# Kernel optimization log

Measured on AMD Instinct MI355X. Metric: run time of the kernel, lower is better.

Reference implementation:

```python
import jax, jax.numpy as jnp
import numpy as np
from jax import lax

DN = ('NHWC', 'HWIO', 'NHWC')


def conv2d(x, w, b):
    y = lax.conv_general_dilated(x, w, window_strides=(1, 1), padding='SAME',
                                 dimension_numbers=DN)
    return y + b


def setup_inputs() -> dict:
    key = jax.random.key(0)
    ks = jax.random.split(key, 9)
    C = 256
    NA, NC = 9, 80
    inp = {
        'x0': jax.random.normal(ks[0], (8, 128, 128, C), jnp.float32),
        'x1': jax.random.normal(ks[1], (8, 64, 64, C), jnp.float32),
        'x2': jax.random.normal(ks[2], (8, 32, 32, C), jnp.float32),
        # 4 intermediate 3x3 conv layers per branch (Conv2DNorm: conv -> relu)
        'cls_w': jax.random.normal(ks[3], (4, 3, 3, C, C), jnp.float32) * 0.05,
        'cls_b': jnp.zeros((4, C), jnp.float32),
        'bbox_w': jax.random.normal(ks[4], (4, 3, 3, C, C), jnp.float32) * 0.05,
        'bbox_b': jnp.zeros((4, C), jnp.float32),
        # final prediction convs (no activation)
        'cls_out_w': jax.random.normal(ks[5], (3, 3, C, NA * NC), jnp.float32) * 0.01,
        'cls_out_b': jnp.full((NA * NC,), -np.log((1 - 0.01) / 0.01), jnp.float32),
        'bbox_out_w': jax.random.normal(ks[6], (3, 3, C, NA * 4), jnp.float32) * 0.01,
        'bbox_out_b': jax.random.normal(ks[7], (NA * 4,), jnp.float32) * 0.01,
    }
    return inp


def _forward_single(x, cls_w, cls_b, bbox_w, bbox_b,
                    cls_out_w, cls_out_b, bbox_out_w, bbox_out_b):
    cls_score = x
    bbox_pred = x
    for i in range(cls_w.shape[0]):  # num_heads = 4, structurally fixed
        cls_score = jax.nn.relu(conv2d(cls_score, cls_w[i], cls_b[i]))
        bbox_pred = jax.nn.relu(conv2d(bbox_pred, bbox_w[i], bbox_b[i]))
    cls_score = conv2d(cls_score, cls_out_w, cls_out_b)
    bbox_pred = conv2d(bbox_pred, bbox_out_w, bbox_out_b)
    return cls_score, bbox_pred


def reference(x0, x1, x2, cls_w, cls_b, bbox_w, bbox_b,
              cls_out_w, cls_out_b, bbox_out_w, bbox_out_b):
    cls_scores, bbox_preds = [], []
    for x in (x0, x1, x2):  # pyramid levels (fixed, structurally distinct shapes)
        c, b = _forward_single(x, cls_w, cls_b, bbox_w, bbox_b,
                               cls_out_w, cls_out_b, bbox_out_w, bbox_out_b)
        cls_scores.append(c)
        bbox_preds.append(b)
    return (*cls_scores, *bbox_preds)
```

## Files before the change

### kernel.cpp

```cpp
#include <hip/hip_runtime.h>
#include <stdint.h>

typedef __attribute__((ext_vector_type(8))) short bf16x8;
typedef __attribute__((ext_vector_type(4))) float f32x4;
typedef __attribute__((ext_vector_type(4))) unsigned int u32x4;

__device__ __forceinline__ unsigned short f2bf(float f) {
  unsigned int u = __float_as_uint(f);
  return (unsigned short)((u + 0x7fffu + ((u >> 16) & 1u)) >> 16);
}

__device__ __forceinline__ void gload16(const void* g, void* l) {
  __builtin_amdgcn_global_load_lds((const __attribute__((address_space(1))) void*)g,
                                   (__attribute__((address_space(3))) void*)l, 16, 0, 0);
}

__global__ void zero_k(u32x4* __restrict__ p, int n16) {
  int i = blockIdx.x * blockDim.x + threadIdx.x;
  int stride = gridDim.x * blockDim.x;
  u32x4 z = {0u, 0u, 0u, 0u};
  for (; i < n16; i += stride) p[i] = z;
}

__global__ void conv_in_k(const float* __restrict__ x, unsigned short* __restrict__ dst,
                          int H, int total) {
  int idx = blockIdx.x * 256 + threadIdx.x;
  if (idx >= total) return;
  const int W = H, Hp = H + 2, Wp = H + 2;
  int c8 = idx & 31;
  int rest = idx >> 5;
  int xp = rest % Wp;
  int r2 = rest / Wp;
  int yp = r2 % Hp;
  int n = r2 / Hp;
  u32x4 o = {0u, 0u, 0u, 0u};
  int iy = yp - 1, ix = xp - 1;
  if ((unsigned)iy < (unsigned)H && (unsigned)ix < (unsigned)W) {
    const float* s = x + ((long)((n * H + iy) * W + ix) * 256 + c8 * 8);
    float4 a = *(const float4*)s;
    float4 b = *(const float4*)(s + 4);
    o.x = f2bf(a.x) | ((unsigned)f2bf(a.y) << 16);
    o.y = f2bf(a.z) | ((unsigned)f2bf(a.w) << 16);
    o.z = f2bf(b.x) | ((unsigned)f2bf(b.y) << 16);
    o.w = f2bf(b.z) | ((unsigned)f2bf(b.w) << 16);
  }
  *(u32x4*)(dst + (long)idx * 8) = o;
}

__global__ void conv_w_k(const float* __restrict__ w, unsigned short* __restrict__ wTf,
                         int CoutReal, int NB, int totalChunks) {
  int f = blockIdx.x * 256 + threadIdx.x;
  if (f >= totalChunks) return;
  int l = f & 63;
  int t2 = f >> 6;
  int ks = t2 & 1;
  int t3 = t2 >> 1;
  int jg = t3 % NB;
  int stage = t3 / NB;
  int col = jg * 16 + (l & 15);
  int kbase = stage * 64 + ks * 32 + ((l >> 4) << 3);
  u32x4 o = {0u, 0u, 0u, 0u};
  if (col < CoutReal) {
    unsigned short v[8];
#pragma unroll
    for (int e = 0; e < 8; ++e)
      v[e] = f2bf(w[(long)(kbase + e) * CoutReal + col]);
    o.x = v[0] | ((unsigned)v[1] << 16);
    o.y = v[2] | ((unsigned)v[3] << 16);
    o.z = v[4] | ((unsigned)v[5] << 16);
    o.w = v[6] | ((unsigned)v[7] << 16);
  }
  *(u32x4*)(wTf + (long)f * 8) = o;
}

template<int NF, bool FINAL>
__global__ __launch_bounds__(256, 2)
void conv3x3_k(const unsigned short* __restrict__ src,
               const unsigned short* __restrict__ wTf,
               const float* __restrict__ bias,
               unsigned short* __restrict__ dstAct,
               float* __restrict__ dstOut,
               int H, int lntx, int lnty, int CoutReal, int NB)
{
  __shared__ char smem[49152];
  const int tid = threadIdx.x;
  const int W = H, Hp = H + 2, RL = H + 2;
  const int np = gridDim.x;
  const int bx = blockIdx.x;
  const int t = (bx & 7) * (np >> 3) + (bx >> 3);
  const int tx = (t & ((1 << lntx) - 1)) << 4;
  const int ty = ((t >> lntx) & ((1 << lnty) - 1)) << 3;
  const int n_img = t >> (lntx + lnty);
  const int tileN = blockIdx.y * (NF * 32);

  int srcOff[6];
#pragma unroll
  for (int j = 0; j < 6; ++j) {
    int q = j * 256 + tid;
    int hr = q >> 3, c = q & 7;
    if (hr >= 180) hr = 0;
    int hy = hr / 18, hx = hr - hy * 18;
    int lch = c ^ (hr & 7);
    srcOff[j] = ((n_img * Hp + ty + hy) * RL + tx + hx) * 256 + lch * 8;
  }

  const int lane = tid & 63;
  const int wv = tid >> 6;
  const int l15 = lane & 15;
  const int k8 = lane >> 4;
  const int pxRow = (wv & 1) * 4;
  const int jgBase = (tileN >> 4) + (wv >> 1) * NF;
  const unsigned short* wBp = wTf + (size_t)jgBase * 1024 + lane * 8;
  const size_t stageStride = (size_t)NB << 10;

  int rBase[4];
#pragma unroll
  for (int m = 0; m < 4; ++m)
    rBase[m] = (pxRow + m) * 18 + l15;

  f32x4 acc[4][NF];
#pragma unroll
  for (int m = 0; m < 4; ++m)
#pragma unroll
    for (int n = 0; n < NF; ++n)
      acc[m][n] = (f32x4){0.f, 0.f, 0.f, 0.f};

  auto loadB = [&](bf16x8 (&dst)[NF][2], int stage) {
    const unsigned short* bp = wBp + stage * stageStride;
#pragma unroll
    for (int n = 0; n < NF; ++n)
#pragma unroll
      for (int ks = 0; ks < 2; ++ks)
        dst[n][ks] = *(const bf16x8*)(bp + n * 1024 + ks * 512);
  };
  auto loadAm = [&](bf16x8 (&dst)[2], const char* buf, int tap, int m) {
    const int ky = tap / 3, kx = tap - ky * 3;
    const int rA = rBase[m] + ky * 18 + kx;
    const int a0 = rA * 128 + ((k8 ^ (rA & 7)) << 4);
    dst[0] = *(const bf16x8*)(buf + a0);
    dst[1] = *(const bf16x8*)(buf + (a0 ^ 64));
  };

  bf16x8 avr[4][2];
  bf16x8 bb[2][NF][2];
  loadB(bb[0], 0);

#pragma unroll
  for (int j = 0; j < 6; ++j)
    gload16(src + srcOff[j], smem + j * 4096 + tid * 16);
  __syncthreads();
#pragma unroll
  for (int m = 0; m < 4; ++m)
    loadAm(avr[m], smem, 0, m);

#pragma unroll
  for (int cc = 0; cc < 4; ++cc) {
    char* cbuf = smem + (cc & 1) * 24576;
    if (cc < 3) {
      char* nbuf = smem + ((cc + 1) & 1) * 24576;
#pragma unroll
      for (int j = 0; j < 6; ++j)
        gload16(src + srcOff[j] + (cc + 1) * 64, nbuf + j * 4096 + tid * 16);
    }
#pragma unroll
    for (int tap = 0; tap < 9; ++tap) {
      const int s = cc * 9 + tap;
      const int cur = s & 1, nxt = cur ^ 1;
      if (cc < 3 || tap < 8)
        loadB(bb[nxt], (tap < 8) ? ((tap + 1) * 4 + cc) : (cc + 1));
      __builtin_amdgcn_s_setprio(1);
#pragma unroll
      for (int m = 0; m < 4; ++m) {
#pragma unroll
        for (int n = 0; n < NF; ++n) {
          acc[m][n] = __builtin_amdgcn_mfma_f32_16x16x32_bf16(avr[m][0], bb[cur][n][0], acc[m][n], 0, 0, 0);
          acc[m][n] = __builtin_amdgcn_mfma_f32_16x16x32_bf16(avr[m][1], bb[cur][n][1], acc[m][n], 0, 0, 0);
        }
        if (tap < 8)
          loadAm(avr[m], cbuf, tap + 1, m);
      }
      __builtin_amdgcn_s_setprio(0);
    }
    __syncthreads();
    if (cc < 3) {
      const char* nbuf = smem + ((cc + 1) & 1) * 24576;
#pragma unroll
      for (int m = 0; m < 4; ++m)
        loadAm(avr[m], nbuf, 0, m);
    }
  }

  if constexpr (FINAL) {
    constexpr int NCOL = NF * 32;
    constexpr int MASK = NCOL / 4 - 1;
    float* cf = (float*)smem;
#pragma unroll
    for (int h = 0; h < 2; ++h) {
      if (h) __syncthreads();
      if ((wv & 1) == h) {
#pragma unroll
        for (int n = 0; n < NF; ++n) {
          const int col = (wv >> 1) * (NF * 16) + n * 16 + l15;
          const int colG = tileN + col;
          const float bvl = (colG < CoutReal) ? bias[colG] : 0.f;
          const int c32 = col >> 2;
#pragma unroll
          for (int m = 0; m < 4; ++m)
#pragma unroll
            for (int r = 0; r < 4; ++r) {
              const int pxl = m * 16 + (k8 << 2) + r;
              const int phys = (c32 + (k8 & 1) * 4) & MASK;
              cf[pxl * NCOL + phys * 4 + (col & 3)] = acc[m][n][r] + bvl;
            }
        }
      }
      __syncthreads();
#pragma unroll
      for (int it = 0; it < NCOL / 16; ++it) {
        const int q = it * 256 + tid;
        const int pxl = q / (NCOL / 4), c32 = q & MASK;
        const int colG = tileN + c32 * 4;
        if (colG < CoutReal) {
          const int phys = (c32 + ((pxl >> 2) & 1) * 4) & MASK;
          u32x4 v = *(const u32x4*)(cf + pxl * NCOL + phys * 4);
          const int px = h * 64 + pxl;
          const int y = ty + (px >> 4), x = tx + (px & 15);
          const size_t p = ((size_t)(n_img * H + y)) * W + x;
          *(u32x4*)(dstOut + p * CoutReal + colG) = v;
        }
      }
    }
  } else {
    unsigned short* cb = (unsigned short*)smem;
#pragma unroll
    for (int n = 0; n < NF; ++n) {
      const int col = (wv >> 1) * (NF * 16) + n * 16 + l15;
      const float bvl = bias[tileN + col];
      const int c16 = col >> 3;
#pragma unroll
      for (int m = 0; m < 4; ++m)
#pragma unroll
        for (int r = 0; r < 4; ++r) {
          const int px = (wv & 1) * 64 + m * 16 + (k8 << 2) + r;
          const int phys = (c16 + k8 * 2) & 15;
          cb[px * 128 + phys * 8 + (col & 7)] = f2bf(fmaxf(acc[m][n][r] + bvl, 0.f));
        }
    }
    __syncthreads();
#pragma unroll
    for (int it = 0; it < 8; ++it) {
      const int q = it * 256 + tid;
      const int px = q >> 4, c16 = q & 15;
      const int phys = (c16 + ((px >> 2) & 3) * 2) & 15;
      u32x4 v = *(const u32x4*)(cb + px * 128 + phys * 8);
      const int y = ty + (px >> 4), x = tx + (px & 15);
      const size_t o = ((size_t)(n_img * Hp + y + 1) * RL + x + 1) * 256 + tileN + c16 * 8;
      *(u32x4*)(dstAct + o) = v;
    }
  }
}

static void run_branch(const unsigned short* A, unsigned short* Am, unsigned short* B,
                       const unsigned short* wT, const float* bias,
                       const unsigned short* wTout, const float* biasOut,
                       bool cls, float* out, int H, int lntx, int lnty,
                       hipStream_t stream) {
  dim3 blk(256);
  const int np = 8 * (H / 16) * (H / 8);
  dim3 g1(np, 2);
  conv3x3_k<4, false><<<g1, blk, 0, stream>>>(A,  wT + 0L * 589824, bias + 0,   B,  nullptr, H, lntx, lnty, 256, 16);
  conv3x3_k<4, false><<<g1, blk, 0, stream>>>(B,  wT + 1L * 589824, bias + 256, Am, nullptr, H, lntx, lnty, 256, 16);
  conv3x3_k<4, false><<<g1, blk, 0, stream>>>(Am, wT + 2L * 589824, bias + 512, B,  nullptr, H, lntx, lnty, 256, 16);
  conv3x3_k<4, false><<<g1, blk, 0, stream>>>(B,  wT + 3L * 589824, bias + 768, Am, nullptr, H, lntx, lnty, 256, 16);
  if (cls) {
    dim3 g2(np, 6);
    conv3x3_k<4, true><<<g2, blk, 0, stream>>>(Am, wTout, biasOut, nullptr, out, H, lntx, lnty, 720, 48);
  } else {
    dim3 g2(np, 1);
    conv3x3_k<2, true><<<g2, blk, 0, stream>>>(Am, wTout, biasOut, nullptr, out, H, lntx, lnty, 36, 4);
  }
}

extern "C" void kernel_launch(void* const* d_in, const int* in_sizes, int n_in,
                              void* d_out, int out_size, void* d_ws, size_t ws_size,
                              hipStream_t stream) {
  const float* x[3] = {(const float*)d_in[0], (const float*)d_in[1], (const float*)d_in[2]};
  const float* cls_w      = (const float*)d_in[3];
  const float* cls_b      = (const float*)d_in[4];
  const float* bbox_w     = (const float*)d_in[5];
  const float* bbox_b     = (const float*)d_in[6];
  const float* cls_out_w  = (const float*)d_in[7];
  const float* cls_out_b  = (const float*)d_in[8];
  const float* bbox_out_w = (const float*)d_in[9];
  const float* bbox_out_b = (const float*)d_in[10];
  float* out = (float*)d_out;

  char* ws = (char*)d_ws;
  unsigned short* bufA = (unsigned short*)ws;
  unsigned short* bufB = (unsigned short*)(ws + 69222400);
  unsigned short* wt   = (unsigned short*)(ws + 138444800);
  unsigned short* wT_cls      = wt;
  unsigned short* wT_bbox     = wt + 4L * 589824;
  unsigned short* wT_cls_out  = wt + 8L * 589824;
  unsigned short* wT_bbox_out = wT_cls_out + 2211840;

  for (int i = 0; i < 4; ++i) {
    conv_w_k<<<288, 256, 0, stream>>>(cls_w  + (long)i * 589824, wT_cls  + (long)i * 589824, 256, 16, 73728);
    conv_w_k<<<288, 256, 0, stream>>>(bbox_w + (long)i * 589824, wT_bbox + (long)i * 589824, 256, 16, 73728);
  }
  conv_w_k<<<864, 256, 0, stream>>>(cls_out_w,  wT_cls_out,  720, 48, 221184);
  conv_w_k<<<72, 256, 0, stream>>>(bbox_out_w, wT_bbox_out, 36, 4, 18432);

  const long clsOff[3] = {0L, 94371840L, 117964800L};
  const long boxOff[3] = {123863040L, 128581632L, 129761280L};
  const int Hs[3]    = {128, 64, 32};
  const int lntxs[3] = {3, 2, 1};
  const int lntys[3] = {4, 3, 2};

  for (int lv = 0; lv < 3; ++lv) {
    const int H = Hs[lv], Hp = H + 2;
    const int paddedElems = 8 * Hp * Hp * 256;
    const int totalConv = 8 * Hp * Hp * 32;

    zero_k<<<2048, 256, 0, stream>>>((u32x4*)bufB, paddedElems / 8);

    conv_in_k<<<(totalConv + 255) / 256, 256, 0, stream>>>(x[lv], bufA, H, totalConv);
    run_branch(bufA, bufA, bufB, wT_cls, cls_b, wT_cls_out, cls_out_b,
               true, out + clsOff[lv], H, lntxs[lv], lntys[lv], stream);

    conv_in_k<<<(totalConv + 255) / 256, 256, 0, stream>>>(x[lv], bufA, H, totalConv);
    run_branch(bufA, bufA, bufB, wT_bbox, bbox_b, wT_bbox_out, bbox_out_b,
               false, out + boxOff[lv], H, lntxs[lv], lntys[lv], stream);
  }
}
```

Measured before the change: 2.040 ms.

## Switch conv MFMA from 16x16x32 to 32x32x16 bf16 with matching weight layout

Replaces the 16x16x32 bf16 MFMA tiles with 32x32x16 tiles. Each wave now computes 2 pixel blocks of 32 by NJ column blocks of 32, and the weight pre-pack layout, LDS A-fragment loads and epilogue index mapping are rewritten to match. The larger MFMA shape gives each wave fewer, larger tiles, which raises arithmetic per loaded fragment and cuts LDS and global read traffic per FLOP. In exchange it changes register pressure and accumulator layout, and adds a barrier before the non-final epilogue.

```diff
diff --git a/kernel.cpp b/kernel.cpp
--- a/kernel.cpp
+++ b/kernel.cpp
@@ -2,7 +2,7 @@
 #include <stdint.h>
 
 typedef __attribute__((ext_vector_type(8))) short bf16x8;
-typedef __attribute__((ext_vector_type(4))) float f32x4;
+typedef __attribute__((ext_vector_type(16))) float f32x16;
 typedef __attribute__((ext_vector_type(4))) unsigned int u32x4;
 
 __device__ __forceinline__ unsigned short f2bf(float f) {
@@ -48,17 +48,17 @@
 }
 
 __global__ void conv_w_k(const float* __restrict__ w, unsigned short* __restrict__ wTf,
-                         int CoutReal, int NB, int totalChunks) {
-  int f = blockIdx.x * 256 + threadIdx.x;
-  if (f >= totalChunks) return;
-  int l = f & 63;
-  int t2 = f >> 6;
-  int ks = t2 & 1;
-  int t3 = t2 >> 1;
-  int jg = t3 % NB;
-  int stage = t3 / NB;
-  int col = jg * 16 + (l & 15);
-  int kbase = stage * 64 + ks * 32 + ((l >> 4) << 3);
+                         int CoutReal, int NB32, int totalThreads) {
+  int idx = blockIdx.x * 256 + threadIdx.x;
+  if (idx >= totalThreads) return;
+  int l = idx & 63;
+  int chunk = idx >> 6;
+  int jg = chunk % NB32;
+  int rest = chunk / NB32;
+  int kstep = rest & 3;
+  int stage = rest >> 2;
+  int col = jg * 32 + (l & 31);
+  int kbase = stage * 64 + kstep * 16 + ((l >> 5) << 3);
   u32x4 o = {0u, 0u, 0u, 0u};
   if (col < CoutReal) {
     unsigned short v[8];
@@ -70,17 +70,17 @@
     o.z = v[4] | ((unsigned)v[5] << 16);
     o.w = v[6] | ((unsigned)v[7] << 16);
   }
-  *(u32x4*)(wTf + (long)f * 8) = o;
-}
-
-template<int NF, bool FINAL>
+  *(u32x4*)(wTf + (long)idx * 8) = o;
+}
+
+template<int NJ, bool FINAL>
 __global__ __launch_bounds__(256, 2)
 void conv3x3_k(const unsigned short* __restrict__ src,
                const unsigned short* __restrict__ wTf,
                const float* __restrict__ bias,
                unsigned short* __restrict__ dstAct,
                float* __restrict__ dstOut,
-               int H, int lntx, int lnty, int CoutReal, int NB)
+               int H, int lntx, int lnty, int CoutReal, int NB32)
 {
   __shared__ char smem[49152];
   const int tid = threadIdx.x;
@@ -91,7 +91,7 @@
   const int tx = (t & ((1 << lntx) - 1)) << 4;
   const int ty = ((t >> lntx) & ((1 << lnty) - 1)) << 3;
   const int n_img = t >> (lntx + lnty);
-  const int tileN = blockIdx.y * (NF * 32);
+  const int tileN = blockIdx.y * (NJ * 64);
 
   int srcOff[6];
 #pragma unroll
@@ -106,43 +106,47 @@
 
   const int lane = tid & 63;
   const int wv = tid >> 6;
-  const int l15 = lane & 15;
-  const int k8 = lane >> 4;
-  const int pxRow = (wv & 1) * 4;
-  const int jgBase = (tileN >> 4) + (wv >> 1) * NF;
-  const unsigned short* wBp = wTf + (size_t)jgBase * 1024 + lane * 8;
-  const size_t stageStride = (size_t)NB << 10;
-
-  int rBase[4];
-#pragma unroll
-  for (int m = 0; m < 4; ++m)
-    rBase[m] = (pxRow + m) * 18 + l15;
-
-  f32x4 acc[4][NF];
-#pragma unroll
-  for (int m = 0; m < 4; ++m)
-#pragma unroll
-    for (int n = 0; n < NF; ++n)
-      acc[m][n] = (f32x4){0.f, 0.f, 0.f, 0.f};
-
-  auto loadB = [&](bf16x8 (&dst)[NF][2], int stage) {
+  const int l31 = lane & 31;
+  const int kh = lane >> 5;
+  const int pxW = (wv & 1) * 64;
+  const int jgW = (tileN >> 5) + (wv >> 1) * NJ;
+  const unsigned short* wBp = wTf + (size_t)jgW * 512 + lane * 8;
+  const size_t stageStride = (size_t)NB32 << 11;
+
+  int rBase[2];
+#pragma unroll
+  for (int m = 0; m < 2; ++m) {
+    const int px = pxW + m * 32 + l31;
+    rBase[m] = (px >> 4) * 18 + (px & 15);
+  }
+
+  f32x16 acc[2][NJ];
+#pragma unroll
+  for (int m = 0; m < 2; ++m)
+#pragma unroll
+    for (int n = 0; n < NJ; ++n)
+      acc[m][n] = (f32x16){0.f};
+
+  auto loadB = [&](bf16x8 (&dst)[NJ][4], int stage) {
     const unsigned short* bp = wBp + stage * stageStride;
 #pragma unroll
-    for (int n = 0; n < NF; ++n)
-#pragma unroll
-      for (int ks = 0; ks < 2; ++ks)
-        dst[n][ks] = *(const bf16x8*)(bp + n * 1024 + ks * 512);
+    for (int jf = 0; jf < NJ; ++jf)
+#pragma unroll
+      for (int ks = 0; ks < 4; ++ks)
+        dst[jf][ks] = *(const bf16x8*)(bp + (ks * NB32 + jf) * 512);
   };
-  auto loadAm = [&](bf16x8 (&dst)[2], const char* buf, int tap, int m) {
+  auto loadAm = [&](bf16x8 (&dst)[4], const char* buf, int tap, int m) {
     const int ky = tap / 3, kx = tap - ky * 3;
     const int rA = rBase[m] + ky * 18 + kx;
-    const int a0 = rA * 128 + ((k8 ^ (rA & 7)) << 4);
-    dst[0] = *(const bf16x8*)(buf + a0);
-    dst[1] = *(const bf16x8*)(buf + (a0 ^ 64));
+    const char* rb = buf + rA * 128;
+    const int sw = rA & 7;
+#pragma unroll
+    for (int ks = 0; ks < 4; ++ks)
+      dst[ks] = *(const bf16x8*)(rb + (((ks * 2 + kh) ^ sw) << 4));
   };
 
-  bf16x8 avr[4][2];
-  bf16x8 bb[2][NF][2];
+  bf16x8 avr[2][4];
+  bf16x8 bb[2][NJ][4];
   loadB(bb[0], 0);
 
 #pragma unroll
@@ -150,7 +154,7 @@
     gload16(src + srcOff[j], smem + j * 4096 + tid * 16);
   __syncthreads();
 #pragma unroll
-  for (int m = 0; m < 4; ++m)
+  for (int m = 0; m < 2; ++m)
     loadAm(avr[m], smem, 0, m);
 
 #pragma unroll
@@ -170,12 +174,13 @@
         loadB(bb[nxt], (tap < 8) ? ((tap + 1) * 4 + cc) : (cc + 1));
       __builtin_amdgcn_s_setprio(1);
 #pragma unroll
-      for (int m = 0; m < 4; ++m) {
-#pragma unroll
-        for (int n = 0; n < NF; ++n) {
-          acc[m][n] = __builtin_amdgcn_mfma_f32_16x16x32_bf16(avr[m][0], bb[cur][n][0], acc[m][n], 0, 0, 0);
-          acc[m][n] = __builtin_amdgcn_mfma_f32_16x16x32_bf16(avr[m][1], bb[cur][n][1], acc[m][n], 0, 0, 0);
-        }
+      for (int m = 0; m < 2; ++m) {
+#pragma unroll
+        for (int ks = 0; ks < 4; ++ks)
+#pragma unroll
+          for (int jf = 0; jf < NJ; ++jf)
+            acc[m][jf] = __builtin_amdgcn_mfma_f32_32x32x16_bf16(
+                avr[m][ks], bb[cur][jf][ks], acc[m][jf], 0, 0, 0);
         if (tap < 8)
           loadAm(avr[m], cbuf, tap + 1, m);
       }
@@ -185,13 +190,13 @@
     if (cc < 3) {
       const char* nbuf = smem + ((cc + 1) & 1) * 24576;
 #pragma unroll
-      for (int m = 0; m < 4; ++m)
+      for (int m = 0; m < 2; ++m)
         loadAm(avr[m], nbuf, 0, m);
     }
   }
 
   if constexpr (FINAL) {
-    constexpr int NCOL = NF * 32;
+    constexpr int NCOL = NJ * 64;
     constexpr int MASK = NCOL / 4 - 1;
     float* cf = (float*)smem;
 #pragma unroll
@@ -199,18 +204,18 @@
       if (h) __syncthreads();
       if ((wv & 1) == h) {
 #pragma unroll
-        for (int n = 0; n < NF; ++n) {
-          const int col = (wv >> 1) * (NF * 16) + n * 16 + l15;
+        for (int jf = 0; jf < NJ; ++jf) {
+          const int col = (wv >> 1) * (NJ * 32) + jf * 32 + l31;
           const int colG = tileN + col;
           const float bvl = (colG < CoutReal) ? bias[colG] : 0.f;
           const int c32 = col >> 2;
 #pragma unroll
-          for (int m = 0; m < 4; ++m)
-#pragma unroll
-            for (int r = 0; r < 4; ++r) {
-              const int pxl = m * 16 + (k8 << 2) + r;
-              const int phys = (c32 + (k8 & 1) * 4) & MASK;
-              cf[pxl * NCOL + phys * 4 + (col & 3)] = acc[m][n][r] + bvl;
+          for (int m = 0; m < 2; ++m)
+#pragma unroll
+            for (int reg = 0; reg < 16; ++reg) {
+              const int pxl = m * 32 + (reg & 3) + 8 * (reg >> 2) + 4 * kh;
+              const int phys = (c32 + ((pxl >> 2) & 1) * 4) & MASK;
+              cf[pxl * NCOL + phys * 4 + (col & 3)] = acc[m][jf][reg] + bvl;
             }
         }
       }
@@ -231,19 +236,21 @@
       }
     }
   } else {
+    __syncthreads();
     unsigned short* cb = (unsigned short*)smem;
 #pragma unroll
-    for (int n = 0; n < NF; ++n) {
-      const int col = (wv >> 1) * (NF * 16) + n * 16 + l15;
+    for (int jf = 0; jf < NJ; ++jf) {
+      const int col = (wv >> 1) * (NJ * 32) + jf * 32 + l31;
       const float bvl = bias[tileN + col];
       const int c16 = col >> 3;
 #pragma unroll
-      for (int m = 0; m < 4; ++m)
-#pragma unroll
-        for (int r = 0; r < 4; ++r) {
-          const int px = (wv & 1) * 64 + m * 16 + (k8 << 2) + r;
-          const int phys = (c16 + k8 * 2) & 15;
-          cb[px * 128 + phys * 8 + (col & 7)] = f2bf(fmaxf(acc[m][n][r] + bvl, 0.f));
+      for (int m = 0; m < 2; ++m)
+#pragma unroll
+        for (int reg = 0; reg < 16; ++reg) {
+          const int px = pxW + m * 32 + (reg & 3) + 8 * (reg >> 2) + 4 * kh;
+          const int phys = (c16 + ((px >> 2) & 3) * 2) & 15;
+          cb[(px & 127) * 128 + phys * 8 + (col & 7)] =
+              f2bf(fmaxf(acc[m][jf][reg] + bvl, 0.f));
         }
     }
     __syncthreads();
@@ -268,16 +275,16 @@
   dim3 blk(256);
   const int np = 8 * (H / 16) * (H / 8);
   dim3 g1(np, 2);
-  conv3x3_k<4, false><<<g1, blk, 0, stream>>>(A,  wT + 0L * 589824, bias + 0,   B,  nullptr, H, lntx, lnty, 256, 16);
-  conv3x3_k<4, false><<<g1, blk, 0, stream>>>(B,  wT + 1L * 589824, bias + 256, Am, nullptr, H, lntx, lnty, 256, 16);
-  conv3x3_k<4, false><<<g1, blk, 0, stream>>>(Am, wT + 2L * 589824, bias + 512, B,  nullptr, H, lntx, lnty, 256, 16);
-  conv3x3_k<4, false><<<g1, blk, 0, stream>>>(B,  wT + 3L * 589824, bias + 768, Am, nullptr, H, lntx, lnty, 256, 16);
+  conv3x3_k<2, false><<<g1, blk, 0, stream>>>(A,  wT + 0L * 589824, bias + 0,   B,  nullptr, H, lntx, lnty, 256, 8);
+  conv3x3_k<2, false><<<g1, blk, 0, stream>>>(B,  wT + 1L * 589824, bias + 256, Am, nullptr, H, lntx, lnty, 256, 8);
+  conv3x3_k<2, false><<<g1, blk, 0, stream>>>(Am, wT + 2L * 589824, bias + 512, B,  nullptr, H, lntx, lnty, 256, 8);
+  conv3x3_k<2, false><<<g1, blk, 0, stream>>>(B,  wT + 3L * 589824, bias + 768, Am, nullptr, H, lntx, lnty, 256, 8);
   if (cls) {
     dim3 g2(np, 6);
-    conv3x3_k<4, true><<<g2, blk, 0, stream>>>(Am, wTout, biasOut, nullptr, out, H, lntx, lnty, 720, 48);
+    conv3x3_k<2, true><<<g2, blk, 0, stream>>>(Am, wTout, biasOut, nullptr, out, H, lntx, lnty, 720, 24);
   } else {
     dim3 g2(np, 1);
-    conv3x3_k<2, true><<<g2, blk, 0, stream>>>(Am, wTout, biasOut, nullptr, out, H, lntx, lnty, 36, 4);
+    conv3x3_k<1, true><<<g2, blk, 0, stream>>>(Am, wTout, biasOut, nullptr, out, H, lntx, lnty, 36, 2);
   }
 }
 
@@ -305,11 +312,11 @@
   unsigned short* wT_bbox_out = wT_cls_out + 2211840;
 
   for (int i = 0; i < 4; ++i) {
-    conv_w_k<<<288, 256, 0, stream>>>(cls_w  + (long)i * 589824, wT_cls  + (long)i * 589824, 256, 16, 73728);
-    conv_w_k<<<288, 256, 0, stream>>>(bbox_w + (long)i * 589824, wT_bbox + (long)i * 589824, 256, 16, 73728);
-  }
-  conv_w_k<<<864, 256, 0, stream>>>(cls_out_w,  wT_cls_out,  720, 48, 221184);
-  conv_w_k<<<72, 256, 0, stream>>>(bbox_out_w, wT_bbox_out, 36, 4, 18432);
+    conv_w_k<<<288, 256, 0, stream>>>(cls_w  + (long)i * 589824, wT_cls  + (long)i * 589824, 256, 8, 73728);
+    conv_w_k<<<288, 256, 0, stream>>>(bbox_w + (long)i * 589824, wT_bbox + (long)i * 589824, 256, 8, 73728);
+  }
+  conv_w_k<<<864, 256, 0, stream>>>(cls_out_w,  wT_cls_out,  720, 24, 221184);
+  conv_w_k<<<72, 256, 0, stream>>>(bbox_out_w, wT_bbox_out, 36, 2, 18432);
 
   const long clsOff[3] = {0L, 94371840L, 117964800L};
   const long boxOff[3] = {123863040L, 128581632L, 129761280L};
```

Result: slower. 2.491 ms (+22.1%).

## Fuse cls and bbox branch conv layers into one launch via grid z

Applied to the files above, without the earlier changes.

Adds a branch index from blockIdx.z so one launch of the intermediate conv kernel processes both the cls and bbox towers, with per-branch source, weight, bias and destination pointers. It picks the buffer plan from workspace size: four buffers for the fused path, three to skip re-converting the input, otherwise the old two-buffer sequence. The fused path doubles the grid per launch and halves the launches, which helps the smaller pyramid levels fill the GPU and removes one input conversion. In exchange it zeroes more buffers and uses a larger workspace.

```diff
diff --git a/kernel.cpp b/kernel.cpp
--- a/kernel.cpp
+++ b/kernel.cpp
@@ -75,10 +75,14 @@
 
 template<int NF, bool FINAL>
 __global__ __launch_bounds__(256, 2)
-void conv3x3_k(const unsigned short* __restrict__ src,
-               const unsigned short* __restrict__ wTf,
-               const float* __restrict__ bias,
-               unsigned short* __restrict__ dstAct,
+void conv3x3_k(const unsigned short* __restrict__ src0,
+               const unsigned short* __restrict__ src1,
+               const unsigned short* __restrict__ wT0,
+               const unsigned short* __restrict__ wT1,
+               const float* __restrict__ bias0,
+               const float* __restrict__ bias1,
+               unsigned short* __restrict__ dstA0,
+               unsigned short* __restrict__ dstA1,
                float* __restrict__ dstOut,
                int H, int lntx, int lnty, int CoutReal, int NB)
 {
@@ -87,6 +91,12 @@
   const int W = H, Hp = H + 2, RL = H + 2;
   const int np = gridDim.x;
   const int bx = blockIdx.x;
+  const int br = blockIdx.z;
+  const unsigned short* src = br ? src1 : src0;
+  const unsigned short* wTf = br ? wT1 : wT0;
+  const float* bias = br ? bias1 : bias0;
+  unsigned short* dstAct = br ? dstA1 : dstA0;
+
   const int t = (bx & 7) * (np >> 3) + (bx >> 3);
   const int tx = (t & ((1 << lntx) - 1)) << 4;
   const int ty = ((t >> lntx) & ((1 << lnty) - 1)) << 3;
@@ -260,24 +270,24 @@
   }
 }
 
-static void run_branch(const unsigned short* A, unsigned short* Am, unsigned short* B,
-                       const unsigned short* wT, const float* bias,
-                       const unsigned short* wTout, const float* biasOut,
-                       bool cls, float* out, int H, int lntx, int lnty,
-                       hipStream_t stream) {
+static void run_branch_seq(const unsigned short* In, unsigned short* B1, unsigned short* B2,
+                           const unsigned short* wT, const float* bias,
+                           const unsigned short* wTout, const float* biasOut,
+                           bool cls, float* out, int H, int lntx, int lnty,
+                           hipStream_t stream) {
   dim3 blk(256);
   const int np = 8 * (H / 16) * (H / 8);
-  dim3 g1(np, 2);
-  conv3x3_k<4, false><<<g1, blk, 0, stream>>>(A,  wT + 0L * 589824, bias + 0,   B,  nullptr, H, lntx, lnty, 256, 16);
-  conv3x3_k<4, false><<<g1, blk, 0, stream>>>(B,  wT + 1L * 589824, bias + 256, Am, nullptr, H, lntx, lnty, 256, 16);
-  conv3x3_k<4, false><<<g1, blk, 0, stream>>>(Am, wT + 2L * 589824, bias + 512, B,  nullptr, H, lntx, lnty, 256, 16);
-  conv3x3_k<4, false><<<g1, blk, 0, stream>>>(B,  wT + 3L * 589824, bias + 768, Am, nullptr, H, lntx, lnty, 256, 16);
+  dim3 g1(np, 2, 1);
+  conv3x3_k<4, false><<<g1, blk, 0, stream>>>(In, In, wT + 0L * 589824, wT, bias, bias, B1, B1, nullptr, H, lntx, lnty, 256, 16);
+  conv3x3_k<4, false><<<g1, blk, 0, stream>>>(B1, B1, wT + 1L * 589824, wT, bias + 256, bias, B2, B2, nullptr, H, lntx, lnty, 256, 16);
+  conv3x3_k<4, false><<<g1, blk, 0, stream>>>(B2, B2, wT + 2L * 589824, wT, bias + 512, bias, B1, B1, nullptr, H, lntx, lnty, 256, 16);
+  conv3x3_k<4, false><<<g1, blk, 0, stream>>>(B1, B1, wT + 3L * 589824, wT, bias + 768, bias, B2, B2, nullptr, H, lntx, lnty, 256, 16);
   if (cls) {
-    dim3 g2(np, 6);
-    conv3x3_k<4, true><<<g2, blk, 0, stream>>>(Am, wTout, biasOut, nullptr, out, H, lntx, lnty, 720, 48);
+    dim3 g2(np, 6, 1);
+    conv3x3_k<4, true><<<g2, blk, 0, stream>>>(B2, B2, wTout, wTout, biasOut, biasOut, nullptr, nullptr, out, H, lntx, lnty, 720, 48);
   } else {
-    dim3 g2(np, 1);
-    conv3x3_k<2, true><<<g2, blk, 0, stream>>>(Am, wTout, biasOut, nullptr, out, H, lntx, lnty, 36, 4);
+    dim3 g2(np, 1, 1);
+    conv3x3_k<2, true><<<g2, blk, 0, stream>>>(B2, B2, wTout, wTout, biasOut, biasOut, nullptr, nullptr, out, H, lntx, lnty, 36, 4);
   }
 }
 
@@ -295,10 +305,17 @@
   const float* bbox_out_b = (const float*)d_in[10];
   float* out = (float*)d_out;
 
+  const size_t BUF = 69222400;
   char* ws = (char*)d_ws;
-  unsigned short* bufA = (unsigned short*)ws;
-  unsigned short* bufB = (unsigned short*)(ws + 69222400);
-  unsigned short* wt   = (unsigned short*)(ws + 138444800);
+  const bool fused  = ws_size >= 4 * BUF + 15000000;
+  const bool triple = !fused && ws_size >= 3 * BUF + 15000000;
+  const int nbuf = fused ? 4 : (triple ? 3 : 2);
+
+  unsigned short* I  = (unsigned short*)ws;
+  unsigned short* B1 = (unsigned short*)(ws + BUF);
+  unsigned short* B2 = (unsigned short*)(ws + 2 * BUF);
+  unsigned short* B3 = (unsigned short*)(ws + 3 * BUF);
+  unsigned short* wt = (unsigned short*)(ws + (size_t)nbuf * BUF);
   unsigned short* wT_cls      = wt;
   unsigned short* wT_bbox     = wt + 4L * 589824;
   unsigned short* wT_cls_out  = wt + 8L * 589824;
@@ -319,17 +336,46 @@
 
   for (int lv = 0; lv < 3; ++lv) {
     const int H = Hs[lv], Hp = H + 2;
+    const int lntx = lntxs[lv], lnty = lntys[lv];
     const int paddedElems = 8 * Hp * Hp * 256;
     const int totalConv = 8 * Hp * Hp * 32;
-
-    zero_k<<<2048, 256, 0, stream>>>((u32x4*)bufB, paddedElems / 8);
-
-    conv_in_k<<<(totalConv + 255) / 256, 256, 0, stream>>>(x[lv], bufA, H, totalConv);
-    run_branch(bufA, bufA, bufB, wT_cls, cls_b, wT_cls_out, cls_out_b,
-               true, out + clsOff[lv], H, lntxs[lv], lntys[lv], stream);
-
-    conv_in_k<<<(totalConv + 255) / 256, 256, 0, stream>>>(x[lv], bufA, H, totalConv);
-    run_branch(bufA, bufA, bufB, wT_bbox, bbox_b, wT_bbox_out, bbox_out_b,
-               false, out + boxOff[lv], H, lntxs[lv], lntys[lv], stream);
-  }
-}
+    const int np = 8 * (H / 16) * (H / 8);
+    dim3 blk(256);
+
+    if (fused) {
+      zero_k<<<2048, 256, 0, stream>>>((u32x4*)B1, paddedElems / 8);
+      zero_k<<<2048, 256, 0, stream>>>((u32x4*)B2, paddedElems / 8);
+      zero_k<<<2048, 256, 0, stream>>>((u32x4*)B3, paddedElems / 8);
+      conv_in_k<<<(totalConv + 255) / 256, 256, 0, stream>>>(x[lv], I, H, totalConv);
+
+      dim3 gf(np, 2, 2);
+      conv3x3_k<4, false><<<gf, blk, 0, stream>>>(I, I, wT_cls + 0L * 589824, wT_bbox + 0L * 589824,
+                                                  cls_b + 0, bbox_b + 0, B1, B2, nullptr, H, lntx, lnty, 256, 16);
+      conv3x3_k<4, false><<<gf, blk, 0, stream>>>(B1, B2, wT_cls + 1L * 589824, wT_bbox + 1L * 589824,
+                                                  cls_b + 256, bbox_b + 256, B3, I, nullptr, H, lntx, lnty, 256, 16);
+      conv3x3_k<4, false><<<gf, blk, 0, stream>>>(B3, I, wT_cls + 2L * 589824, wT_bbox + 2L * 589824,
+                                                  cls_b + 512, bbox_b + 512, B1, B2, nullptr, H, lntx, lnty, 256, 16);
+      conv3x3_k<4, false><<<gf, blk, 0, stream>>>(B1, B2, wT_cls + 3L * 589824, wT_bbox + 3L * 589824,
+                                                  cls_b + 768, bbox_b + 768, B3, I, nullptr, H, lntx, lnty, 256, 16);
+      dim3 gc(np, 6, 1);
+      conv3x3_k<4, true><<<gc, blk, 0, stream>>>(B3, B3, wT_cls_out, wT_cls_out, cls_out_b, cls_out_b,
+                                                 nullptr, nullptr, out + clsOff[lv], H, lntx, lnty, 720, 48);
+      dim3 gb(np, 1, 1);
+      conv3x3_k<2, true><<<gb, blk, 0, stream>>>(I, I, wT_bbox_out, wT_bbox_out, bbox_out_b, bbox_out_b,
+                                                 nullptr, nullptr, out + boxOff[lv], H, lntx, lnty, 36, 4);
+    } else {
+      unsigned short* pB2 = triple ? B2 : I;
+      zero_k<<<2048, 256, 0, stream>>>((u32x4*)B1, paddedElems / 8);
+      if (triple)
+        zero_k<<<2048, 256, 0, stream>>>((u32x4*)B2, paddedElems / 8);
+
+      conv_in_k<<<(totalConv + 255) / 256, 256, 0, stream>>>(x[lv], I, H, totalConv);
+      run_branch_seq(I, B1, pB2, wT_cls, cls_b, wT_cls_out, cls_out_b,
+                     true, out + clsOff[lv], H, lntx, lnty, stream);
+      if (!triple)
+        conv_in_k<<<(totalConv + 255) / 256, 256, 0, stream>>>(x[lv], I, H, totalConv);
+      run_branch_seq(I, B1, pB2, wT_bbox, bbox_b, wT_bbox_out, bbox_out_b,
+                     false, out + boxOff[lv], H, lntx, lnty, stream);
+    }
+  }
+}
```

Result: faster. 1.985 ms (-2.7%).
